# Performance work log

Hardware: AMD Instinct MI355X
Metric: run time of the kernel (lower is better)

Reference implementation:

```python
import jax, jax.numpy as jnp
import numpy as np

N, E = 50000, 800000
D_IN, NH, F_OUT = 128, 8, 32
HID, D_EMB, BINS = 256, 64, 200


def setup_inputs() -> dict:
    key = jax.random.key(0)
    ks = jax.random.split(key, 16)
    inp = {
        "node_features": jax.random.normal(ks[0], (N, D_IN), jnp.float32),
        "edge_src": jax.random.randint(ks[1], (E,), 0, N),
        "edge_trg": jax.random.randint(ks[2], (E,), 0, N),
        "edge_dist_bins": jax.random.randint(ks[3], (E,), 0, BINS),
        "moving_state": jax.random.normal(ks[4], (HID,), jnp.float32),
        "li": 123,
        "ld": 4567,
        "distance": 77,
        # GAT params
        "Wproj": jax.random.normal(ks[5], (NH * F_OUT, D_IN), jnp.float32) / np.sqrt(D_IN),
        "a_src": jax.random.normal(ks[6], (NH, F_OUT), jnp.float32) * 0.1,
        "a_trg": jax.random.normal(ks[7], (NH, F_OUT), jnp.float32) * 0.1,
        "Wms": jax.random.normal(ks[8], (NH, HID), jnp.float32) / np.sqrt(HID),
        "dist_emb_gat": jax.random.normal(ks[9], (BINS, D_EMB), jnp.float32) * 0.1,
        "Wdist": jax.random.normal(ks[10], (NH, D_EMB), jnp.float32) / np.sqrt(D_EMB),
        "Wskip": jax.random.normal(ks[11], (NH * F_OUT, D_IN), jnp.float32) / np.sqrt(D_IN),
        "gat_bias": jnp.zeros((F_OUT,), jnp.float32),
        # FunctionH params: input = hidden + F_OUT + F_OUT + D_EMB
        "dist_emb_h": jax.random.normal(ks[12], (BINS, D_EMB), jnp.float32) * 0.1,
        "W1": jax.random.normal(ks[13], (HID, HID + 2 * F_OUT + D_EMB), jnp.float32) / np.sqrt(HID + 2 * F_OUT + D_EMB),
        "b1": jnp.zeros((HID,), jnp.float32),
        "W2": jax.random.normal(ks[14], (1, HID), jnp.float32) / np.sqrt(HID),
        "b2": jnp.zeros((1,), jnp.float32),
    }
    return inp


def gat_forward(node_features, moving_state, edge_src, edge_trg, edge_dist_bins,
                Wproj, a_src, a_trg, Wms, dist_emb_gat, Wdist, Wskip, gat_bias):
    # project: (N, NH, F)
    proj = (node_features @ Wproj.T).reshape(N, NH, F_OUT)
    s_src = jnp.einsum("nhf,hf->nh", proj, a_src)  # (N, NH)
    s_trg = jnp.einsum("nhf,hf->nh", proj, a_trg)  # (N, NH)
    s_ms = Wms @ moving_state                       # (NH,)
    e_score = dist_emb_gat[edge_dist_bins] @ Wdist.T  # (E, NH)
    scores = jax.nn.leaky_relu(s_src[edge_src] + s_trg[edge_trg] + s_ms + e_score, 0.2)
    # neighborhood-aware softmax (Imp3: global max for stability, per-trg sums)
    exp_s = jnp.exp(scores - jax.lax.stop_gradient(scores.max()))
    denom = jax.ops.segment_sum(exp_s, edge_trg, num_segments=N)  # (N, NH)
    attn = exp_s / (denom[edge_trg] + 1e-16)                      # (E, NH)
    weighted = proj[edge_src] * attn[:, :, None]                  # (E, NH, F)
    out = jax.ops.segment_sum(weighted, edge_trg, num_segments=N)  # (N, NH, F)
    # skip connection (dims differ -> skip_proj), then head-average, bias, ELU
    out = out + (node_features @ Wskip.T).reshape(N, NH, F_OUT)
    out = out.mean(axis=1) + gat_bias  # (N, F)
    return jax.nn.elu(out)


def reference(node_features, edge_src, edge_trg, edge_dist_bins, moving_state,
              li, ld, distance,
              Wproj, a_src, a_trg, Wms, dist_emb_gat, Wdist, Wskip, gat_bias,
              dist_emb_h, W1, b1, W2, b2):
    node_emb = gat_forward(node_features, moving_state, edge_src, edge_trg, edge_dist_bins,
                           Wproj, a_src, a_trg, Wms, dist_emb_gat, Wdist, Wskip, gat_bias)
    feat = jnp.concatenate([moving_state, node_emb[li], node_emb[ld], dist_emb_h[distance]], axis=0)
    h1 = jax.nn.relu(W1 @ feat + b1)
    return W2 @ h1 + b2  # (1,)
```

## Files before the change

kernel.cpp:

```cpp
#include <hip/hip_runtime.h>
#include <hip/hip_bf16.h>
#include <math.h>

#define D_IN  128
#define NH    8
#define F_OUT 32
#define HID   256
#define D_EMB 64
#define BINS  200
#define FDIM  384
#define CAP   128
#define SLOTS 6

#define NSCANB 219
#define VSRC_B 219
#define SKIP_B 227
#define ESC_B  235
#define SMS_B  239
#define PRE1_B 240
#define K1GRID 256
#define K2GRID 32

#define AR __ATOMIC_RELAXED
#define SA __HIP_MEMORY_SCOPE_AGENT
#define STF(p, v) __hip_atomic_store((p), (v), AR, SA)
#define LDF(p)    __hip_atomic_load((p), AR, SA)


__device__ __forceinline__ float redw(float v) {
#pragma unroll
  for (int o = 32; o > 0; o >>= 1) v += __shfl_down(v, o, 64);
  return v;
}

__device__ __forceinline__ void vm0() {
  asm volatile("s_waitcnt vmcnt(0)" ::: "memory");
}

__global__ __launch_bounds__(512, 1) void scan_pre_k(
    const float* __restrict__ nf, const int* __restrict__ esrc,
    const int* __restrict__ etrg, const int* __restrict__ ebin,
    const float* __restrict__ ms, const int* __restrict__ li_p,
    const int* __restrict__ ld_p, const int* __restrict__ dist_p,
    const float* __restrict__ Wproj, const float* __restrict__ a_src,
    const float* __restrict__ a_trg, const float* __restrict__ Wms,
    const float* __restrict__ demb_g, const float* __restrict__ Wdist,
    const float* __restrict__ Wskip, const float* __restrict__ W1,
    const float* __restrict__ b1, const float* __restrict__ demb_h,
    int nE, int* __restrict__ ws_i, float* __restrict__ fb) {
  int* bcnt = ws_i + 16;
  int* bsrc = ws_i + 256;
  int* btrg = ws_i + 1600;
  int* bbin = ws_i + 2944;
  float* vsrc   = fb;
  float* strg   = fb + 1024;
  float* sms    = fb + 1040;
  float* escall = fb + 1048;
  float* skipb  = fb + 2648;
  float* pre1   = fb + 3160;
  float* bnf    = fb + 4096;

  __shared__ __align__(16) float s_nf2[2 * D_IN];
  __shared__ __align__(16) float s_vp[2][4][D_IN];
  __shared__ int l_cnt;
  __shared__ int l_src[SLOTS], l_trg[SLOTS], l_bin[SLOTS];

  const int bid = blockIdx.x, tid = threadIdx.x;
  const int wv = tid >> 6, ln = tid & 63;
  const int li = li_p[0], ld = ld_p[0];

  if (bid < NSCANB) {
    if (tid == 0) l_cnt = 0;
    __syncthreads();
    const int gid = bid * 512 + tid;
    const int stride = NSCANB * 512;
    const int nE4 = nE >> 2;
    const int4* t4 = (const int4*)etrg;
    for (int e4 = gid; e4 < nE4; e4 += stride) {
      int4 t = t4[e4];
      int ev[4] = {t.x, t.y, t.z, t.w};
#pragma unroll
      for (int k = 0; k < 4; ++k) {
        if (ev[k] == li || ev[k] == ld) {
          int e = e4 * 4 + k;
          int p = atomicAdd(&l_cnt, 1);
          if (p < SLOTS) { l_src[p] = esrc[e]; l_trg[p] = ev[k]; l_bin[p] = ebin[e]; }
        }
      }
    }
    if (bid == 0 && tid == 0) {
      for (int e = nE4 * 4; e < nE; ++e) {
        int tv = etrg[e];
        if (tv == li || tv == ld) {
          int p = atomicAdd(&l_cnt, 1);
          if (p < SLOTS) { l_src[p] = esrc[e]; l_trg[p] = tv; l_bin[p] = ebin[e]; }
        }
      }
    }
    __syncthreads();
    int c = l_cnt; if (c > SLOTS) c = SLOTS;
    if (tid == 0) bcnt[bid] = c;
    if (tid < c) {
      bsrc[bid * SLOTS + tid] = l_src[tid];
      btrg[bid * SLOTS + tid] = l_trg[tid];
      bbin[bid * SLOTS + tid] = l_bin[tid];
    }
    if (wv < c && ln < 32)
      ((float4*)(bnf + (size_t)(bid * SLOTS + wv) * D_IN))[ln] =
          ((const float4*)(nf + (size_t)l_src[wv] * D_IN))[ln];
    return;
  }

  if (bid < SKIP_B) {
    const int h = bid - VSRC_B;
    if (h == 0 && tid == 0) { ws_i[0] = 0; ws_i[1] = 0; }
    const int d = tid & 127, fg = tid >> 7;
    float as = 0.f, at = 0.f;
    for (int f = fg * 8; f < fg * 8 + 8; ++f) {
      float w = Wproj[(h * F_OUT + f) * D_IN + d];
      as = fmaf(a_src[h * F_OUT + f], w, as);
      at = fmaf(a_trg[h * F_OUT + f], w, at);
    }
    s_vp[0][fg][d] = as; s_vp[1][fg][d] = at;
    __syncthreads();
    if (tid < 128)
      vsrc[h * D_IN + tid] =
          s_vp[0][0][tid] + s_vp[0][1][tid] + s_vp[0][2][tid] + s_vp[0][3][tid];
    if (tid >= 128 && tid < 256) {
      int dd = tid - 128;
      s_vp[1][0][dd] = s_vp[1][0][dd] + s_vp[1][1][dd] + s_vp[1][2][dd] + s_vp[1][3][dd];
    }
    if (tid >= 256 && tid < 320) {
      int j = tid - 256;
      ((float4*)s_nf2)[j] = ((const float4*)(nf + (size_t)(j < 32 ? li : ld) * D_IN))[j & 31];
    }
    __syncthreads();
    if (wv < 2) {
      float part = s_nf2[wv * D_IN + ln * 2] * s_vp[1][0][ln * 2]
                 + s_nf2[wv * D_IN + ln * 2 + 1] * s_vp[1][0][ln * 2 + 1];
      part = redw(part);
      if (ln == 0) strg[wv * NH + h] = part;
    }
  } else if (bid < ESC_B) {
    const int base = (bid - SKIP_B) * 32;
    if (tid < 64)
      ((float4*)s_nf2)[tid] = ((const float4*)(nf + (size_t)(tid < 32 ? li : ld) * D_IN))[tid & 31];
    __syncthreads();
    for (int rd = 0; rd < 4; ++rd) {
      int r = base + rd * 8 + wv;
      float w0 = Wskip[r * D_IN + ln * 2], w1 = Wskip[r * D_IN + ln * 2 + 1];
      float o0 = w0 * s_nf2[ln * 2] + w1 * s_nf2[ln * 2 + 1];
      float o1 = w0 * s_nf2[D_IN + ln * 2] + w1 * s_nf2[D_IN + ln * 2 + 1];
      o0 = redw(o0); o1 = redw(o1);
      if (ln == 0) { skipb[r] = o0; skipb[256 + r] = o1; }
    }
  } else if (bid < SMS_B) {
    const int p = bid - ESC_B;
    const int g = tid >> 3, l8 = tid & 7;
    for (int it = g; it < 50 * NH; it += 64) {
      int bin = p * 50 + (it >> 3), hh = it & 7;
      const float* de = demb_g + bin * D_EMB + l8 * 8;
      const float* wd = Wdist + hh * D_EMB + l8 * 8;
      float a = 0.f;
#pragma unroll
      for (int j = 0; j < 8; ++j) a = fmaf(de[j], wd[j], a);
#pragma unroll
      for (int o = 4; o > 0; o >>= 1) a += __shfl_down(a, o, 8);
      if (l8 == 0) escall[bin * NH + hh] = a;
    }
  } else if (bid < PRE1_B) {
    const float* wr = Wms + wv * HID;
    float a = 0.f;
#pragma unroll
    for (int m = 0; m < 4; ++m) a = fmaf(wr[ln + 64 * m], ms[ln + 64 * m], a);
    a = redw(a);
    if (ln == 0) sms[wv] = a;
  } else {
    const int q = bid - PRE1_B;
    const int dist = dist_p[0];
    for (int rr = 0; rr < 2; ++rr) {
      int r = q * 16 + wv * 2 + rr;
      const float* w = W1 + (size_t)r * FDIM;
      float a = 0.f;
#pragma unroll
      for (int m = 0; m < 4; ++m) a = fmaf(w[ln + 64 * m], ms[ln + 64 * m], a);
      a = fmaf(w[320 + ln], demb_h[(size_t)dist * D_EMB + ln], a);
      a = redw(a);
      if (ln == 0) pre1[r] = a + b1[r];
    }
  }
}

__global__ __launch_bounds__(512, 1) void finalize_k(
    const int* __restrict__ li_p,
    const float* __restrict__ Wproj, const float* __restrict__ gbias,
    const float* __restrict__ W1, const float* __restrict__ W2,
    const float* __restrict__ b2,
    int* __restrict__ ws_i, float* __restrict__ fb, float* __restrict__ out) {
  int* flag_proj = ws_i;
  int* flag_mlp  = ws_i + 1;
  int* bcnt = ws_i + 16;
  int* btrg = ws_i + 1600;
  int* bbin = ws_i + 2944;
  float* vsrc    = fb;
  float* strg    = fb + 1024;
  float* sms     = fb + 1040;
  float* escall  = fb + 1048;
  float* skipb   = fb + 2648;
  float* pre1    = fb + 3160;
  float* out_ws  = fb + 3416;
  float* partial = fb + 3928;
  float* bnf     = fb + 4096;

  __shared__ int   s_tot;
  __shared__ int   s_sl[CAP], s_tb[CAP], s_bn[CAP];
  __shared__ float s_p[CAP];
  __shared__ float s_den[2];
  __shared__ __align__(16) float s_vs[D_IN];
  __shared__ __align__(16) float s_agg[2][D_IN];
  __shared__ __align__(16) float s_out[512];
  __shared__ __align__(16) float s_emb[64];
  __shared__ float s_pr[8];

  const int k = blockIdx.x, tid = threadIdx.x;
  const int wv = tid >> 6, ln = tid & 63;
  const int li = li_p[0];
  const int h = k >> 2;
  const int row = k * 8 + wv;

  const float wpA = Wproj[row * D_IN + ln * 2];
  const float wpB = Wproj[row * D_IN + ln * 2 + 1];
  const float w1e = W1[(size_t)row * FDIM + HID + ln];
  const float w2v = W2[row];

  if (tid == 0) s_tot = 0;
  __syncthreads();
  if (tid < NSCANB) {
    int c = bcnt[tid];
    if (c > 0) {
      if (c > SLOTS) c = SLOTS;
      int base = atomicAdd(&s_tot, c);
      for (int j = 0; j < c; ++j)
        if (base + j < CAP) s_sl[base + j] = tid * SLOTS + j;
    }
  }
  __syncthreads();
  int cnt = s_tot; if (cnt > CAP) cnt = CAP;
  if (tid < cnt) {
    int sl = s_sl[tid];
    s_tb[tid] = (btrg[sl] == li) ? 0 : 1;
    s_bn[tid] = bbin[sl];
  }
  if (tid < D_IN) s_vs[tid] = vsrc[h * D_IN + tid];
  __syncthreads();
  const float sms_h = sms[h], strg0 = strg[h], strg1 = strg[NH + h];

  for (int e = wv; e < cnt; e += 8) {
    const float* nfr = bnf + (size_t)s_sl[e] * D_IN + ln * 2;
    float part = nfr[0] * s_vs[ln * 2] + nfr[1] * s_vs[ln * 2 + 1];
    part = redw(part);
    if (ln == 0) {
      float sc = part + (s_tb[e] ? strg1 : strg0) + sms_h + escall[s_bn[e] * NH + h];
      sc = sc > 0.f ? sc : 0.2f * sc;
      s_p[e] = expf(sc);
    }
  }
  __syncthreads();
  if (tid < 2) {
    float d = 1e-16f;
    for (int e = 0; e < cnt; ++e) if (s_tb[e] == (int)tid) d += s_p[e];
    s_den[tid] = d;
  }
  __syncthreads();
  if (tid < cnt) s_p[tid] = s_p[tid] / s_den[s_tb[tid]];
  __syncthreads();
  if (tid < 256) {
    const int t = tid >> 7, d = tid & 127;
    float a = 0.f;
    for (int e = 0; e < cnt; ++e)
      if (s_tb[e] == t) a = fmaf(s_p[e], bnf[(size_t)s_sl[e] * D_IN + d], a);
    s_agg[t][d] = a;
  }
  __syncthreads();
  {
    float o0 = wpA * s_agg[0][ln * 2] + wpB * s_agg[0][ln * 2 + 1];
    float o1 = wpA * s_agg[1][ln * 2] + wpB * s_agg[1][ln * 2 + 1];
    o0 = redw(o0); o1 = redw(o1);
    if (ln == 0) {
      STF(out_ws + row,       o0 + skipb[row]);
      STF(out_ws + 256 + row, o1 + skipb[256 + row]);
    }
  }
  vm0();
  __syncthreads();
  if (tid == 0) {
    __hip_atomic_fetch_add(flag_proj, 1, AR, SA);
    while (LDF(flag_proj) < K2GRID) __builtin_amdgcn_s_sleep(1);
  }
  __syncthreads();

  s_out[tid] = LDF(out_ws + tid);
  __syncthreads();
  if (tid < 64) {
    const int t = tid >> 5, f = tid & 31;
    float s = 0.f;
#pragma unroll
    for (int hh = 0; hh < NH; ++hh) s += s_out[t * 256 + hh * F_OUT + f];
    s = s * 0.125f + gbias[f];
    s_emb[tid] = s > 0.f ? s : expm1f(s);
  }
  __syncthreads();
  {
    float acc = redw(w1e * s_emb[ln]);
    if (ln == 0) {
      float h1 = fmaxf(pre1[row] + acc, 0.f);
      s_pr[wv] = w2v * h1;
    }
  }
  __syncthreads();
  if (tid == 0) {
    float bp = 0.f;
#pragma unroll
    for (int w = 0; w < 8; ++w) bp += s_pr[w];
    STF(partial + k, bp);
    vm0();
    int ret = __hip_atomic_fetch_add(flag_mlp, 1, AR, SA);
    if (ret == K2GRID - 1) {
      float s = b2[0];
      for (int j = 0; j < K2GRID; ++j) s += LDF(partial + j);
      out[0] = s;
    }
  }
}

extern "C" void kernel_launch(void* const* d_in, const int* in_sizes, int n_in,
                              void* d_out, int out_size, void* d_ws, size_t ws_size,
                              hipStream_t stream) {
  const float* nf     = (const float*)d_in[0];
  const int*   esrc   = (const int*)d_in[1];
  const int*   etrg   = (const int*)d_in[2];
  const int*   ebin   = (const int*)d_in[3];
  const float* ms     = (const float*)d_in[4];
  const int*   li_p   = (const int*)d_in[5];
  const int*   ld_p   = (const int*)d_in[6];
  const int*   dist_p = (const int*)d_in[7];
  const float* Wproj  = (const float*)d_in[8];
  const float* a_src  = (const float*)d_in[9];
  const float* a_trg  = (const float*)d_in[10];
  const float* Wms    = (const float*)d_in[11];
  const float* demb_g = (const float*)d_in[12];
  const float* Wdist  = (const float*)d_in[13];
  const float* Wskip  = (const float*)d_in[14];
  const float* gbias  = (const float*)d_in[15];
  const float* demb_h = (const float*)d_in[16];
  const float* W1     = (const float*)d_in[17];
  const float* b1     = (const float*)d_in[18];
  const float* W2     = (const float*)d_in[19];
  const float* b2     = (const float*)d_in[20];
  const int nE = in_sizes[1];

  int*   ws_i = (int*)d_ws;
  float* fb   = (float*)d_ws + 8192;

  scan_pre_k<<<K1GRID, 512, 0, stream>>>(
      nf, esrc, etrg, ebin, ms, li_p, ld_p, dist_p,
      Wproj, a_src, a_trg, Wms, demb_g, Wdist, Wskip, W1, b1, demb_h,
      nE, ws_i, fb);

  finalize_k<<<K2GRID, 512, 0, stream>>>(
      li_p, Wproj, gbias, W1, W2, b2, ws_i, fb, (float*)d_out);
}
```

Measured before the change: 26.65 us.

## Shrink finalize grid to one block per head and stage gathered rows in LDS

Result: no change. 27.10 us (+1.7%).

```diff
diff --git a/kernel.cpp b/kernel.cpp
--- a/kernel.cpp
+++ b/kernel.cpp
@@ -11,6 +11,8 @@
 #define FDIM  384
 #define CAP   128
 #define SLOTS 6
+#define SNF   64
+#define NSLOT (219 * SLOTS)
 
 #define NSCANB 219
 #define VSRC_B 219
@@ -19,7 +21,7 @@
 #define SMS_B  239
 #define PRE1_B 240
 #define K1GRID 256
-#define K2GRID 32
+#define K2GRID 8
 
 #define AR __ATOMIC_RELAXED
 #define SA __HIP_MEMORY_SCOPE_AGENT
@@ -113,7 +115,7 @@
 
   if (bid < SKIP_B) {
     const int h = bid - VSRC_B;
-    if (h == 0 && tid == 0) { ws_i[0] = 0; ws_i[1] = 0; }
+    if (h == 0 && tid < 16) ws_i[tid] = 0;
     const int d = tid & 127, fg = tid >> 7;
     float as = 0.f, at = 0.f;
     for (int f = fg * 8; f < fg * 8 + 8; ++f) {
@@ -197,8 +199,8 @@
     const float* __restrict__ W1, const float* __restrict__ W2,
     const float* __restrict__ b2,
     int* __restrict__ ws_i, float* __restrict__ fb, float* __restrict__ out) {
-  int* flag_proj = ws_i;
-  int* flag_mlp  = ws_i + 1;
+  int* flag_mlp  = ws_i;
+  int* done_proj = ws_i + 8;
   int* bcnt = ws_i + 16;
   int* btrg = ws_i + 1600;
   int* bbin = ws_i + 2944;
@@ -212,55 +214,88 @@
   float* partial = fb + 3928;
   float* bnf     = fb + 4096;
 
-  __shared__ int   s_tot;
-  __shared__ int   s_sl[CAP], s_tb[CAP], s_bn[CAP];
+  __shared__ int s_bc[256], s_sc[256];
+  __shared__ int s_mt[NSLOT], s_mb[NSLOT];
+  __shared__ int s_sl[CAP], s_tb[CAP], s_bn[CAP];
   __shared__ float s_p[CAP];
   __shared__ float s_den[2];
   __shared__ __align__(16) float s_vs[D_IN];
+  __shared__ float s_eh[BINS];
+  __shared__ float s_sk0[32], s_sk1[32], s_p1[32];
+  __shared__ float s_3[3];
+  __shared__ __align__(16) float s_bnf[SNF * D_IN];
   __shared__ __align__(16) float s_agg[2][D_IN];
   __shared__ __align__(16) float s_out[512];
   __shared__ __align__(16) float s_emb[64];
   __shared__ float s_pr[8];
 
-  const int k = blockIdx.x, tid = threadIdx.x;
+  const int h = blockIdx.x, tid = threadIdx.x;
   const int wv = tid >> 6, ln = tid & 63;
   const int li = li_p[0];
-  const int h = k >> 2;
-  const int row = k * 8 + wv;
-
-  const float wpA = Wproj[row * D_IN + ln * 2];
-  const float wpB = Wproj[row * D_IN + ln * 2 + 1];
-  const float w1e = W1[(size_t)row * FDIM + HID + ln];
-  const float w2v = W2[row];
-
-  if (tid == 0) s_tot = 0;
-  __syncthreads();
+
+  float wpA[4], wpB[4], w1e[4], w2v[4];
+#pragma unroll
+  for (int j = 0; j < 4; ++j) {
+    const int r = h * 32 + wv * 4 + j;
+    wpA[j] = Wproj[r * D_IN + ln * 2];
+    wpB[j] = Wproj[r * D_IN + ln * 2 + 1];
+    w1e[j] = W1[(size_t)r * FDIM + HID + ln];
+    w2v[j] = W2[r];
+  }
+  if (tid < 256) s_bc[tid] = (tid < NSCANB) ? bcnt[tid] : 0;
+  for (int i = tid; i < NSLOT; i += 512) { s_mt[i] = btrg[i]; s_mb[i] = bbin[i]; }
+  if (tid < D_IN) s_vs[tid] = vsrc[h * D_IN + tid];
+  if (tid < BINS) s_eh[tid] = escall[tid * NH + h];
+  if (tid < 32) {
+    s_sk0[tid] = skipb[h * 32 + tid];
+    s_sk1[tid] = skipb[256 + h * 32 + tid];
+    s_p1[tid]  = pre1[h * 32 + tid];
+  }
+  if (tid < 3) s_3[tid] = (tid == 0) ? sms[h] : strg[(tid - 1) * NH + h];
+  __syncthreads();
+
+  if (tid < 256) s_sc[tid] = s_bc[tid];
+  __syncthreads();
+  for (int off = 1; off < 256; off <<= 1) {
+    int v = 0;
+    if (tid < 256 && tid >= off) v = s_sc[tid - off];
+    __syncthreads();
+    if (tid < 256) s_sc[tid] += v;
+    __syncthreads();
+  }
+  int cnt = s_sc[255]; if (cnt > CAP) cnt = CAP;
   if (tid < NSCANB) {
-    int c = bcnt[tid];
-    if (c > 0) {
-      if (c > SLOTS) c = SLOTS;
-      int base = atomicAdd(&s_tot, c);
-      for (int j = 0; j < c; ++j)
-        if (base + j < CAP) s_sl[base + j] = tid * SLOTS + j;
-    }
-  }
-  __syncthreads();
-  int cnt = s_tot; if (cnt > CAP) cnt = CAP;
+    int c = s_bc[tid], base = s_sc[tid] - c;
+    for (int j = 0; j < c; ++j)
+      if (base + j < CAP) s_sl[base + j] = tid * SLOTS + j;
+  }
+  __syncthreads();
   if (tid < cnt) {
     int sl = s_sl[tid];
-    s_tb[tid] = (btrg[sl] == li) ? 0 : 1;
-    s_bn[tid] = bbin[sl];
-  }
-  if (tid < D_IN) s_vs[tid] = vsrc[h * D_IN + tid];
-  __syncthreads();
-  const float sms_h = sms[h], strg0 = strg[h], strg1 = strg[NH + h];
-
+    s_tb[tid] = (s_mt[sl] == li) ? 0 : 1;
+    s_bn[tid] = s_mb[sl];
+  }
+  __syncthreads();
+
+  {
+    const int lim = (cnt < SNF ? cnt : SNF) * 32;
+    float4* dst = (float4*)s_bnf;
+    for (int i4 = tid; i4 < lim; i4 += 512)
+      dst[i4] = ((const float4*)bnf)[(size_t)s_sl[i4 >> 5] * 32 + (i4 & 31)];
+  }
+  __syncthreads();
+
+  const float sms_h = s_3[0], strg0 = s_3[1], strg1 = s_3[2];
   for (int e = wv; e < cnt; e += 8) {
-    const float* nfr = bnf + (size_t)s_sl[e] * D_IN + ln * 2;
-    float part = nfr[0] * s_vs[ln * 2] + nfr[1] * s_vs[ln * 2 + 1];
-    part = redw(part);
+    float x0, x1;
+    if (e < SNF) { x0 = s_bnf[e * D_IN + ln * 2]; x1 = s_bnf[e * D_IN + ln * 2 + 1]; }
+    else {
+      const float* g = bnf + (size_t)s_sl[e] * D_IN + ln * 2;
+      x0 = g[0]; x1 = g[1];
+    }
+    float part = redw(x0 * s_vs[ln * 2] + x1 * s_vs[ln * 2 + 1]);
     if (ln == 0) {
-      float sc = part + (s_tb[e] ? strg1 : strg0) + sms_h + escall[s_bn[e] * NH + h];
+      float sc = part + (s_tb[e] ? strg1 : strg0) + sms_h + s_eh[s_bn[e]];
       sc = sc > 0.f ? sc : 0.2f * sc;
       s_p[e] = expf(sc);
     }
@@ -277,26 +312,32 @@
   if (tid < 256) {
     const int t = tid >> 7, d = tid & 127;
     float a = 0.f;
-    for (int e = 0; e < cnt; ++e)
-      if (s_tb[e] == t) a = fmaf(s_p[e], bnf[(size_t)s_sl[e] * D_IN + d], a);
+    for (int e = 0; e < cnt; ++e) {
+      if (s_tb[e] == t) {
+        float v = (e < SNF) ? s_bnf[e * D_IN + d] : bnf[(size_t)s_sl[e] * D_IN + d];
+        a = fmaf(s_p[e], v, a);
+      }
+    }
     s_agg[t][d] = a;
   }
   __syncthreads();
-  {
-    float o0 = wpA * s_agg[0][ln * 2] + wpB * s_agg[0][ln * 2 + 1];
-    float o1 = wpA * s_agg[1][ln * 2] + wpB * s_agg[1][ln * 2 + 1];
+
+#pragma unroll
+  for (int j = 0; j < 4; ++j) {
+    const int r = h * 32 + wv * 4 + j;
+    float o0 = wpA[j] * s_agg[0][ln * 2] + wpB[j] * s_agg[0][ln * 2 + 1];
+    float o1 = wpA[j] * s_agg[1][ln * 2] + wpB[j] * s_agg[1][ln * 2 + 1];
     o0 = redw(o0); o1 = redw(o1);
     if (ln == 0) {
-      STF(out_ws + row,       o0 + skipb[row]);
-      STF(out_ws + 256 + row, o1 + skipb[256 + row]);
+      STF(out_ws + r,       o0 + s_sk0[wv * 4 + j]);
+      STF(out_ws + 256 + r, o1 + s_sk1[wv * 4 + j]);
     }
   }
   vm0();
   __syncthreads();
-  if (tid == 0) {
-    __hip_atomic_fetch_add(flag_proj, 1, AR, SA);
-    while (LDF(flag_proj) < K2GRID) __builtin_amdgcn_s_sleep(1);
-  }
+  if (tid == 0) STF(done_proj + h, 1);
+  if (tid < K2GRID)
+    while (LDF(done_proj + tid) == 0) __builtin_amdgcn_s_sleep(1);
   __syncthreads();
 
   s_out[tid] = LDF(out_ws + tid);
@@ -311,18 +352,23 @@
   }
   __syncthreads();
   {
-    float acc = redw(w1e * s_emb[ln]);
-    if (ln == 0) {
-      float h1 = fmaxf(pre1[row] + acc, 0.f);
-      s_pr[wv] = w2v * h1;
-    }
+    float bp = 0.f;
+#pragma unroll
+    for (int j = 0; j < 4; ++j) {
+      float acc = redw(w1e[j] * s_emb[ln]);
+      if (ln == 0) {
+        float h1 = fmaxf(s_p1[wv * 4 + j] + acc, 0.f);
+        bp += w2v[j] * h1;
+      }
+    }
+    if (ln == 0) s_pr[wv] = bp;
   }
   __syncthreads();
   if (tid == 0) {
     float bp = 0.f;
 #pragma unroll
     for (int w = 0; w < 8; ++w) bp += s_pr[w];
-    STF(partial + k, bp);
+    STF(partial + h, bp);
     vm0();
     int ret = __hip_atomic_fetch_add(flag_mlp, 1, AR, SA);
     if (ret == K2GRID - 1) {
```
